# Kernel tuning notes

Measured on AMD Instinct MI355X. Metric: run time of the kernel, lower is better.

The kernel has to match this reference:

```python
import jax, jax.numpy as jnp
import numpy as np


def fwht(x):
    """Normalized fast Walsh-Hadamard transform along last dim (== matmul_hadU).
    x[..., n] with n a power of 2; returns H_n @ x / sqrt(n) (Sylvester ordering).
    """
    orig_shape = x.shape
    n = orig_shape[-1]
    x = x.reshape(-1, n)
    h = 1
    while h < n:
        # pair elements at distance h: butterfly (a+b, a-b)
        x = x.reshape(-1, n // (2 * h), 2, h)
        a = x[:, :, 0:1, :]
        b = x[:, :, 1:2, :]
        x = jnp.concatenate([a + b, a - b], axis=2).reshape(-1, n)
        h *= 2
    scale = jnp.asarray(1.0 / np.sqrt(n), x.dtype)
    return (x * scale).reshape(orig_shape)


def setup_inputs() -> dict:
    key = jax.random.key(0)
    k1, k2, k3 = jax.random.split(key, 3)
    B, S, D_IN, D_OUT = 4, 2048, 4096, 4096
    x = jax.random.normal(k1, (B, S, D_IN), dtype=jnp.float32)
    W = jax.random.normal(k2, (D_OUT, D_IN), dtype=jnp.float32) * (1.0 / np.sqrt(D_IN))
    b = jax.random.normal(k3, (D_OUT,), dtype=jnp.float32)
    return {"x": x, "W": W, "b": b}


def reference(x, W, b):
    # Hadamard rotation of the activations, then Linear: y = fwht(x) @ W.T + b
    rotated = fwht(x)                                   # [B, S, D_in]
    return jnp.einsum("bsd,od->bso", rotated, W) + b    # [B, S, D_out]
```

## Files before the change

kernel.cpp:

```cpp
#include <hip/hip_runtime.h>
#include <hip/hip_bf16.h>
#include <cstdint>
#include <cstddef>

typedef __bf16 bf16_t;
typedef bf16_t bf16x4 __attribute__((ext_vector_type(4)));
typedef bf16_t bf16x8 __attribute__((ext_vector_type(8)));
typedef float  f32x4  __attribute__((ext_vector_type(4)));

#define FWHT_N 4096
#define BM 128
#define BN 128
#define BK 32

__global__ __launch_bounds__(256) void fwht_rows_bf16(const float* __restrict__ W,
                                                      bf16_t* __restrict__ Wt) {
    __shared__ float row[FWHT_N];
    const int r   = blockIdx.x;
    const int tid = threadIdx.x;

    const float4* src  = (const float4*)(W + (size_t)r * FWHT_N);
    float4*       rowv = (float4*)row;
#pragma unroll
    for (int i = 0; i < 4; ++i) rowv[tid + 256 * i] = src[tid + 256 * i];
    __syncthreads();

    for (int h = 1; h < FWHT_N; h <<= 1) {
#pragma unroll
        for (int it = 0; it < 8; ++it) {
            const int p = tid + 256 * it;
            const int i = ((p & ~(h - 1)) << 1) | (p & (h - 1));
            const float a = row[i];
            const float b = row[i + h];
            row[i]     = a + b;
            row[i + h] = a - b;
        }
        __syncthreads();
    }

    const float s = 0.015625f;
    bf16x4* dst = (bf16x4*)(Wt + (size_t)r * FWHT_N);
#pragma unroll
    for (int i = 0; i < 4; ++i) {
        const float4 v = rowv[tid + 256 * i];
        bf16x4 o;
        o[0] = (bf16_t)(v.x * s);
        o[1] = (bf16_t)(v.y * s);
        o[2] = (bf16_t)(v.z * s);
        o[3] = (bf16_t)(v.w * s);
        dst[tid + 256 * i] = o;
    }
}

__global__ __launch_bounds__(256) void cvt_f32_bf16(const float4* __restrict__ x,
                                                    bf16x4* __restrict__ y) {
    const size_t i = (size_t)blockIdx.x * 256 + threadIdx.x;
    const float4 v = x[i];
    bf16x4 o;
    o[0] = (bf16_t)v.x;
    o[1] = (bf16_t)v.y;
    o[2] = (bf16_t)v.z;
    o[3] = (bf16_t)v.w;
    y[i] = o;
}

__device__ __forceinline__ void g2lds16(const bf16_t* g, bf16_t* l) {
    __builtin_amdgcn_global_load_lds((__attribute__((address_space(1))) void*)g,
                                     (__attribute__((address_space(3))) void*)l,
                                     16, 0, 0);
}

__global__ __launch_bounds__(256) void gemm_bt_bias(const bf16_t* __restrict__ A,
                                                    const bf16_t* __restrict__ Bm,
                                                    const float* __restrict__ bias,
                                                    float* __restrict__ C,
                                                    int M, int N, int K) {
    __shared__ __align__(16) bf16_t As[BM * BK];
    __shared__ __align__(16) bf16_t Bs[BN * BK];

    const int tid  = threadIdx.x;
    const int wave = tid >> 6;
    const int lane = tid & 63;
    const int quad = lane >> 4;
    const int l16  = lane & 15;

    const int bn = blockIdx.x;
    const int bm = blockIdx.y;
    const int m0 = bm * BM;
    const int n0 = bn * BN;

    const int wm = (wave >> 1) * 64;
    const int wn = (wave & 1) * 64;

    const int ldrow = tid >> 2;
    const int ldcol = (tid & 3) * 8;

    const bf16_t* gA = A  + (size_t)(m0 + ldrow) * K + ldcol;
    const bf16_t* gB = Bm + (size_t)(n0 + ldrow) * K + ldcol;
    const size_t half = (size_t)64 * K;

    bf16_t* lA = &As[tid * 8];
    bf16_t* lB = &Bs[tid * 8];

    f32x4 acc[4][4] = {};

    for (int k0 = 0; k0 < K; k0 += BK) {
        g2lds16(gA,        lA);
        g2lds16(gA + half, lA + 2048);
        g2lds16(gB,        lB);
        g2lds16(gB + half, lB + 2048);
        gA += BK;
        gB += BK;
        __syncthreads();

        bf16x8 af[4], bfr[4];
#pragma unroll
        for (int mi = 0; mi < 4; ++mi)
            af[mi] = *(const bf16x8*)&As[(wm + mi * 16 + l16) * BK + quad * 8];
#pragma unroll
        for (int ni = 0; ni < 4; ++ni)
            bfr[ni] = *(const bf16x8*)&Bs[(wn + ni * 16 + l16) * BK + quad * 8];

#pragma unroll
        for (int mi = 0; mi < 4; ++mi)
#pragma unroll
            for (int ni = 0; ni < 4; ++ni)
                acc[mi][ni] = __builtin_amdgcn_mfma_f32_16x16x32_bf16(
                    af[mi], bfr[ni], acc[mi][ni], 0, 0, 0);

        __syncthreads();
    }

    const int crow = quad * 4;
#pragma unroll
    for (int ni = 0; ni < 4; ++ni) {
        const int n  = n0 + wn + ni * 16 + l16;
        const float bv = bias[n];
#pragma unroll
        for (int mi = 0; mi < 4; ++mi) {
            const int mb = m0 + wm + mi * 16 + crow;
#pragma unroll
            for (int r = 0; r < 4; ++r)
                C[(size_t)(mb + r) * N + n] = acc[mi][ni][r] + bv;
        }
    }
}

extern "C" void kernel_launch(void* const* d_in, const int* in_sizes, int n_in,
                              void* d_out, int out_size, void* d_ws, size_t ws_size,
                              hipStream_t stream) {
    const float* x = (const float*)d_in[0];
    const float* W = (const float*)d_in[1];
    const float* b = (const float*)d_in[2];
    float* out = (float*)d_out;

    const int K = 4096;
    const int N = 4096;
    const int M = in_sizes[0] / K;

    bf16_t* xb = (bf16_t*)d_ws;
    bf16_t* Wt = xb + (size_t)M * K;

    hipLaunchKernelGGL(fwht_rows_bf16, dim3(N), dim3(256), 0, stream, W, Wt);

    const int cvt_blocks = (int)(((size_t)M * K) / 4 / 256);
    hipLaunchKernelGGL(cvt_f32_bf16, dim3(cvt_blocks), dim3(256), 0, stream,
                       (const float4*)x, (bf16x4*)xb);

    hipLaunchKernelGGL(gemm_bt_bias, dim3(N / BN, M / BM), dim3(256), 0, stream,
                       xb, Wt, b, out, M, N, K);
}
```

Before: 611.4 us.

## Register-blocked radix-16 FWHT with padded LDS and wider bf16 conversion

The row FWHT on W goes from 12 LDS passes with a barrier after each to three radix-16 stages done in registers, joined by two padded shared-memory transposes. This is meant to cut LDS traffic and synchronisation in the weight transform. The conversion kernel also now handles 8 floats per thread and writes bf16x8. The final FWHT store writes scalar bf16 at stride 256, which makes the global writes less coalesced.

```diff
diff --git a/kernel.cpp b/kernel.cpp
--- a/kernel.cpp
+++ b/kernel.cpp
@@ -13,54 +13,73 @@
 #define BN 128
 #define BK 32
 
-__global__ __launch_bounds__(256) void fwht_rows_bf16(const float* __restrict__ W,
-                                                      bf16_t* __restrict__ Wt) {
-    __shared__ float row[FWHT_N];
-    const int r   = blockIdx.x;
-    const int tid = threadIdx.x;
-
-    const float4* src  = (const float4*)(W + (size_t)r * FWHT_N);
-    float4*       rowv = (float4*)row;
+__device__ __forceinline__ void fwht16(float v[16]) {
 #pragma unroll
-    for (int i = 0; i < 4; ++i) rowv[tid + 256 * i] = src[tid + 256 * i];
-    __syncthreads();
-
-    for (int h = 1; h < FWHT_N; h <<= 1) {
+    for (int h = 1; h < 16; h <<= 1) {
 #pragma unroll
-        for (int it = 0; it < 8; ++it) {
-            const int p = tid + 256 * it;
-            const int i = ((p & ~(h - 1)) << 1) | (p & (h - 1));
-            const float a = row[i];
-            const float b = row[i + h];
-            row[i]     = a + b;
-            row[i + h] = a - b;
+        for (int i = 0; i < 16; ++i) {
+            if (!(i & h)) {
+                const float a = v[i];
+                const float b = v[i | h];
+                v[i]     = a + b;
+                v[i | h] = a - b;
+            }
         }
-        __syncthreads();
-    }
-
-    const float s = 0.015625f;
-    bf16x4* dst = (bf16x4*)(Wt + (size_t)r * FWHT_N);
-#pragma unroll
-    for (int i = 0; i < 4; ++i) {
-        const float4 v = rowv[tid + 256 * i];
-        bf16x4 o;
-        o[0] = (bf16_t)(v.x * s);
-        o[1] = (bf16_t)(v.y * s);
-        o[2] = (bf16_t)(v.z * s);
-        o[3] = (bf16_t)(v.w * s);
-        dst[tid + 256 * i] = o;
     }
 }
 
+__device__ __forceinline__ int pad(int i) { return i + (i >> 5); }
+
+__global__ __launch_bounds__(256) void fwht_rows_bf16(const float* __restrict__ W,
+                                                      bf16_t* __restrict__ Wt) {
+    __shared__ float lds[FWHT_N + (FWHT_N >> 5)];
+    const int r = blockIdx.x;
+    const int t = threadIdx.x;
+
+    float v[16];
+
+    const float4* src = (const float4*)(W + (size_t)r * FWHT_N + 16 * t);
+    {
+        const float4 a0 = src[0], a1 = src[1], a2 = src[2], a3 = src[3];
+        v[0] = a0.x; v[1] = a0.y; v[2]  = a0.z; v[3]  = a0.w;
+        v[4] = a1.x; v[5] = a1.y; v[6]  = a1.z; v[7]  = a1.w;
+        v[8] = a2.x; v[9] = a2.y; v[10] = a2.z; v[11] = a2.w;
+        v[12] = a3.x; v[13] = a3.y; v[14] = a3.z; v[15] = a3.w;
+    }
+    fwht16(v);
+    {
+        const int base = 16 * t + (t >> 1);
+#pragma unroll
+        for (int k = 0; k < 16; ++k) lds[base + k] = v[k];
+    }
+    __syncthreads();
+
+    const int b1 = ((t >> 4) << 8) | (t & 15);
+#pragma unroll
+    for (int k = 0; k < 16; ++k) v[k] = lds[pad(b1 + (k << 4))];
+    fwht16(v);
+#pragma unroll
+    for (int k = 0; k < 16; ++k) lds[pad(b1 + (k << 4))] = v[k];
+    __syncthreads();
+
+#pragma unroll
+    for (int k = 0; k < 16; ++k) v[k] = lds[pad(t + (k << 8))];
+    fwht16(v);
+
+    const float s = 0.015625f;
+    bf16_t* dst = Wt + (size_t)r * FWHT_N + t;
+#pragma unroll
+    for (int k = 0; k < 16; ++k) dst[k << 8] = (bf16_t)(v[k] * s);
+}
+
 __global__ __launch_bounds__(256) void cvt_f32_bf16(const float4* __restrict__ x,
-                                                    bf16x4* __restrict__ y) {
+                                                    bf16x8* __restrict__ y) {
     const size_t i = (size_t)blockIdx.x * 256 + threadIdx.x;
-    const float4 v = x[i];
-    bf16x4 o;
-    o[0] = (bf16_t)v.x;
-    o[1] = (bf16_t)v.y;
-    o[2] = (bf16_t)v.z;
-    o[3] = (bf16_t)v.w;
+    const float4 a = x[2 * i];
+    const float4 b = x[2 * i + 1];
+    bf16x8 o;
+    o[0] = (bf16_t)a.x; o[1] = (bf16_t)a.y; o[2] = (bf16_t)a.z; o[3] = (bf16_t)a.w;
+    o[4] = (bf16_t)b.x; o[5] = (bf16_t)b.y; o[6] = (bf16_t)b.z; o[7] = (bf16_t)b.w;
     y[i] = o;
 }
 
@@ -163,9 +182,9 @@
 
     hipLaunchKernelGGL(fwht_rows_bf16, dim3(N), dim3(256), 0, stream, W, Wt);
 
-    const int cvt_blocks = (int)(((size_t)M * K) / 4 / 256);
+    const int cvt_blocks = (int)(((size_t)M * K) / 8 / 256);
     hipLaunchKernelGGL(cvt_f32_bf16, dim3(cvt_blocks), dim3(256), 0, stream,
-                       (const float4*)x, (bf16x4*)xb);
+                       (const float4*)x, (bf16x8*)xb);
 
     hipLaunchKernelGGL(gemm_bt_bias, dim3(N / BN, M / BM), dim3(256), 0, stream,
                        xb, Wt, b, out, M, N, K);
```

Result: no change. 609.2 us (-0.4%).
